# Performance work log

Hardware: AMD Instinct MI355X
Metric: run time of the kernel (lower is better)

Reference implementation:

```python
import jax, jax.numpy as jnp
import numpy as np

D_MODEL = 1024
N_LAYERS = 2
D_STATE = 16
D_CONV = 4
D_INNER = 2 * D_MODEL          # mamba expand=2
DT_RANK = 64                   # ceil(d_model/16)
EPS = 1e-5


def rmsnorm(x, w, eps=EPS):
    return x * jax.lax.rsqrt(jnp.mean(x * x, axis=-1, keepdims=True) + eps) * w


def silu(x):
    return x * jax.nn.sigmoid(x)


def selective_scan(u, dt, A, B, C, Dp):
    # u, dt: (b,l,d)  A: (d,n)  B,C: (b,l,n)  Dp: (d,)
    b, l, d = u.shape
    n = A.shape[1]

    def step(h, inp):
        u_t, dt_t, B_t, C_t = inp          # (b,d),(b,d),(b,n),(b,n)
        dA = jnp.exp(dt_t[..., None] * A)  # (b,d,n)
        h = dA * h + (dt_t * u_t)[..., None] * B_t[:, None, :]
        y = jnp.einsum('bdn,bn->bd', h, C_t)
        return h, y

    h0 = jnp.zeros((b, d, n), u.dtype)
    xs = (u.transpose(1, 0, 2), dt.transpose(1, 0, 2),
          B.transpose(1, 0, 2), C.transpose(1, 0, 2))
    _, ys = jax.lax.scan(step, h0, xs)
    return ys.transpose(1, 0, 2) + u * Dp


def mamba_mixer(x, in_w, conv_w, conv_b, xp_w, dt_w, dt_b, A_log, Dp, out_w):
    b, l, _ = x.shape
    xz = jnp.einsum('bld,ed->ble', x, in_w)        # (b,l,2*d_inner)
    xi, z = jnp.split(xz, 2, axis=-1)
    # depthwise causal conv1d, kernel D_CONV
    xp = jnp.pad(xi, ((0, 0), (D_CONV - 1, 0), (0, 0)))
    xc = conv_b + sum(xp[:, k:k + l, :] * conv_w[:, k] for k in range(D_CONV))
    xc = silu(xc)
    dbc = jnp.einsum('bld,ed->ble', xc, xp_w)      # (b,l,dt_rank+2n)
    dt_low = dbc[..., :DT_RANK]
    Bm = dbc[..., DT_RANK:DT_RANK + D_STATE]
    Cm = dbc[..., DT_RANK + D_STATE:]
    dt = jax.nn.softplus(jnp.einsum('blr,dr->bld', dt_low, dt_w) + dt_b)
    A = -jnp.exp(A_log)
    y = selective_scan(xc, dt, A, Bm, Cm, Dp)
    y = y * silu(z)
    return jnp.einsum('bld,od->blo', y, out_w)


def setup_inputs() -> dict:
    key = jax.random.key(0)
    ks = jax.random.split(key, 8)
    s = 0.02
    hidden_states = jax.random.normal(ks[0], (1, 2048, D_MODEL), jnp.float32)
    norm_w = jnp.ones((N_LAYERS, D_MODEL), jnp.float32)
    in_proj_w = jax.random.normal(ks[1], (N_LAYERS, 2 * D_INNER, D_MODEL), jnp.float32) * s
    conv_w = jax.random.normal(ks[2], (N_LAYERS, D_INNER, D_CONV), jnp.float32) * 0.2
    conv_b = jnp.zeros((N_LAYERS, D_INNER), jnp.float32)
    x_proj_w = jax.random.normal(ks[3], (N_LAYERS, DT_RANK + 2 * D_STATE, D_INNER), jnp.float32) * s
    dt_proj_w = jax.random.normal(ks[4], (N_LAYERS, D_INNER, DT_RANK), jnp.float32) * (DT_RANK ** -0.5)
    # softplus^{-1}(0.01) ~= -4.6 (mamba dt bias init regime)
    dt_proj_b = jnp.full((N_LAYERS, D_INNER), -4.6, jnp.float32) + \
        jax.random.normal(ks[5], (N_LAYERS, D_INNER), jnp.float32) * 0.1
    A_log = jnp.log(jnp.broadcast_to(
        jnp.arange(1, D_STATE + 1, dtype=jnp.float32), (N_LAYERS, D_INNER, D_STATE)))
    D_param = jnp.ones((N_LAYERS, D_INNER), jnp.float32)
    out_proj_w = jax.random.normal(ks[6], (N_LAYERS, D_MODEL, D_INNER), jnp.float32) * s
    norm_f_w = jnp.ones((D_MODEL,), jnp.float32)
    return {
        'hidden_states': hidden_states, 'norm_w': norm_w, 'in_proj_w': in_proj_w,
        'conv_w': conv_w, 'conv_b': conv_b, 'x_proj_w': x_proj_w,
        'dt_proj_w': dt_proj_w, 'dt_proj_b': dt_proj_b, 'A_log': A_log,
        'D_param': D_param, 'out_proj_w': out_proj_w, 'norm_f_w': norm_f_w,
    }


def reference(hidden_states, norm_w, in_proj_w, conv_w, conv_b, x_proj_w,
              dt_proj_w, dt_proj_b, A_log, D_param, out_proj_w, norm_f_w):
    h = hidden_states
    residual = None
    for i in range(N_LAYERS):
        # fused add + RMSNorm (prenorm): residual accumulates the stream
        residual = h if residual is None else h + residual
        hn = rmsnorm(residual, norm_w[i])
        h = mamba_mixer(hn, in_proj_w[i], conv_w[i], conv_b[i], x_proj_w[i],
                        dt_proj_w[i], dt_proj_b[i], A_log[i], D_param[i], out_proj_w[i])
    # final fused add + RMSNorm (prenorm=False)
    return rmsnorm(h + residual, norm_f_w)
```

## Files before the change

### kernel.cpp

```cpp
#include <hip/hip_runtime.h>
#include <math.h>

#define D_MODEL 1024
#define D_INNER 2048
#define DPROJ   96
#define DT_RANK 64
#define NSTATE  16
#define SEQ     2048
#define CL      16
#define NCH     (SEQ/CL)
#define SCAN_SEGS 4
#define SCAN_CPS  (NCH / SCAN_SEGS)
#define LOG2E   1.44269504088896340736f

typedef unsigned short ushort_t;
typedef short v8s __attribute__((ext_vector_type(8)));
typedef unsigned short u8s __attribute__((ext_vector_type(8)));
typedef float v4f __attribute__((ext_vector_type(4)));
typedef __attribute__((address_space(3))) unsigned int as3_u32;
typedef __attribute__((address_space(1))) unsigned int as1_u32;

__device__ __forceinline__ float silu_f(float x) { return x / (1.f + expf(-x)); }

__device__ __forceinline__ ushort_t f2bf(float f) {
  union { float f; unsigned u; } x; x.f = f;
  unsigned r = x.u + 0x7fffu + ((x.u >> 16) & 1u);
  return (ushort_t)(r >> 16);
}
__device__ __forceinline__ float bf2f(ushort_t b) {
  union { unsigned u; float f; } x; x.u = ((unsigned)b) << 16; return x.f;
}

__device__ __forceinline__ void gl_lds16(const ushort_t* g, ushort_t* l) {
  __builtin_amdgcn_global_load_lds((const as1_u32*)g, (as3_u32*)l, 16, 0, 0);
}

__global__ __launch_bounds__(256) void addrms_kernel(
    const float* __restrict__ a, const float* __restrict__ a2,
    const float* __restrict__ a3, const float* __restrict__ a4,
    const float* __restrict__ b,
    const float* __restrict__ w, float* __restrict__ res_out,
    float* __restrict__ xnf, ushort_t* __restrict__ xnb) {
  int t = blockIdx.x;
  int tid = threadIdx.x;
  float v[4];
  float ss = 0.f;
#pragma unroll
  for (int j = 0; j < 4; ++j) {
    int dcol = tid + j * 256;
    size_t off = (size_t)t * D_MODEL + dcol;
    float x = a[off];
    if (a2) x += a2[off];
    if (a3) x += a3[off];
    if (a4) x += a4[off];
    if (b) x += b[off];
    v[j] = x;
    ss += x * x;
  }
#pragma unroll
  for (int off = 32; off > 0; off >>= 1) ss += __shfl_down(ss, off);
  __shared__ float red[4];
  __shared__ float rmsv;
  int wid = tid >> 6, lane = tid & 63;
  if (lane == 0) red[wid] = ss;
  __syncthreads();
  if (tid == 0) {
    float s = red[0] + red[1] + red[2] + red[3];
    rmsv = rsqrtf(s / (float)D_MODEL + 1e-5f);
  }
  __syncthreads();
  float r = rmsv;
#pragma unroll
  for (int j = 0; j < 4; ++j) {
    int dcol = tid + j * 256;
    if (res_out) res_out[(size_t)t * D_MODEL + dcol] = v[j];
    float xn = v[j] * r * w[dcol];
    if (xnf) xnf[(size_t)t * D_MODEL + dcol] = xn;
    if (xnb) xnb[(size_t)t * D_MODEL + dcol] = f2bf(xn);
  }
}

__global__ __launch_bounds__(256) void f2bf_all_kernel(
    const float* __restrict__ s0, ushort_t* __restrict__ d0, int n0,
    const float* __restrict__ s1, ushort_t* __restrict__ d1, int n1,
    const float* __restrict__ s2, ushort_t* __restrict__ d2, int n2,
    const float* __restrict__ s3, ushort_t* __restrict__ d3, int n3) {
  int j = blockIdx.x * 256 + threadIdx.x;
  const float* s; ushort_t* d;
  if (j < n0) { s = s0; d = d0; }
  else {
    j -= n0;
    if (j < n1) { s = s1; d = d1; }
    else {
      j -= n1;
      if (j < n2) { s = s2; d = d2; }
      else {
        j -= n2;
        if (j >= n3) return;
        s = s3; d = d3;
      }
    }
  }
  float4 v = ((const float4*)s)[j];
  ushort4 o;
  o.x = f2bf(v.x); o.y = f2bf(v.y); o.z = f2bf(v.z); o.w = f2bf(v.w);
  ((ushort4*)d)[j] = o;
}

template <int SPLITK, bool CLAMPN, int EPI>
__global__ __launch_bounds__(256) void gemm_bt(
    const ushort_t* __restrict__ A, const ushort_t* __restrict__ B,
    void* __restrict__ Cv, const float* __restrict__ bias,
    const ushort_t* __restrict__ upack,
    int M, int N, int K, int lda, int ldb, int ldc) {
  __shared__ ushort_t As[2][128 * 32];
  __shared__ ushort_t Bs[2][128 * 32];
  int tid = threadIdx.x;

  int gx = gridDim.x, gy = gridDim.y;
  int nwg = gx * gy * gridDim.z;
  int phys = blockIdx.x + gx * (blockIdx.y + gy * blockIdx.z);
  int q = nwg >> 3, r = nwg & 7;
  int xcd = phys & 7, idx8 = phys >> 3;
  int lbid = (xcd < r ? xcd * (q + 1) : r * (q + 1) + (xcd - r) * q) + idx8;
  int bx = lbid % gx, by = (lbid / gx) % gy, bz = lbid / (gx * gy);

  int bm = by * 128;
  int bn = bx * 128;
  int kchunk = K / SPLITK;
  int k0 = bz * kchunk;
  int nk = kchunk / 32;

  int lane = tid & 63, wid = tid >> 6;
  int wr = wid >> 1, wc = wid & 1;
  int lr = lane & 15;
  int ko = (lane >> 4) * 8;

  int rs0 = wid * 16 + (lane >> 2);
  int segc = (lane & 3) * 8;

  auto stage = [&](int buf, int kt) {
#pragma unroll
    for (int s = 0; s < 2; ++s) {
      int r2 = s * 64 + rs0;
      int cc = kt + segc;
      gl_lds16(A + (size_t)(bm + r2) * lda + cc, &As[buf][s * 2048 + wid * 512]);
      int bc = bn + r2;
      if (CLAMPN) bc = min(bc, N - 1);
      gl_lds16(B + (size_t)bc * ldb + cc, &Bs[buf][s * 2048 + wid * 512]);
    }
  };

  v4f acc[4][4] = {};

  stage(0, k0);
  __syncthreads();
  int cur = 0;
  for (int it = 0; it < nk; ++it) {
    if (it + 1 < nk) stage(cur ^ 1, k0 + (it + 1) * 32);
    v8s a[4], b[4];
#pragma unroll
    for (int m = 0; m < 4; ++m)
      a[m] = *(const v8s*)&As[cur][(wr * 64 + m * 16 + lr) * 32 + ko];
#pragma unroll
    for (int n = 0; n < 4; ++n)
      b[n] = *(const v8s*)&Bs[cur][(wc * 64 + n * 16 + lr) * 32 + ko];
#pragma unroll
    for (int m = 0; m < 4; ++m)
#pragma unroll
      for (int n = 0; n < 4; ++n)
        acc[m][n] = __builtin_amdgcn_mfma_f32_16x16x32_bf16(a[m], b[n], acc[m][n], 0, 0, 0);
    __syncthreads();
    cur ^= 1;
  }

  float* Cf = (float*)Cv;
  ushort_t* Cb = (ushort_t*)Cv;
  unsigned* Cu = (unsigned*)Cv;
  if (SPLITK > 1) Cf += (size_t)bz * (size_t)M * (size_t)ldc;

#pragma unroll
  for (int m = 0; m < 4; ++m) {
#pragma unroll
    for (int n = 0; n < 4; ++n) {
      int gc = bn + wc * 64 + n * 16 + lr;
      if (gc >= N) continue;
      int gr0 = bm + wr * 64 + m * 16 + (lane >> 4) * 4;
      float bv = (EPI == 1 || EPI == 3) ? bias[gc] : 0.f;
#pragma unroll
      for (int j = 0; j < 4; ++j) {
        float val = acc[m][n][j];
        size_t idx = (size_t)(gr0 + j) * ldc + gc;
        if (EPI == 0) {
          Cf[idx] = val;
        } else if (EPI == 1) {
          float x = val + bv;
          x = fmaxf(x, 0.f) + log1pf(expf(-fabsf(x)));
          Cb[idx] = f2bf(x);
        } else if (EPI == 2) {
          Cb[idx] = f2bf(val);
        } else {
          float x = val + bv;
          x = fmaxf(x, 0.f) + log1pf(expf(-fabsf(x)));
          Cu[idx] = (unsigned)f2bf(x) | ((unsigned)upack[idx] << 16);
        }
      }
    }
  }
}

__global__ __launch_bounds__(256) void reduceN_kernel(
    const float* __restrict__ part, float* __restrict__ out,
    ushort_t* __restrict__ outb, int sz, int nparts) {
  int idx = blockIdx.x * 256 + threadIdx.x;
  if (idx >= sz) return;
  float s = 0.f;
  for (int p = 0; p < nparts; ++p) s += part[idx + (size_t)p * sz];
  if (out) out[idx] = s;
  if (outb) outb[idx] = f2bf(s);
}

__global__ __launch_bounds__(256) void conv_silu_kernel(
    const ushort_t* __restrict__ xzb, const float* __restrict__ cw,
    const float* __restrict__ cb, ushort_t* __restrict__ xcb) {
  int idx = blockIdx.x * 256 + threadIdx.x;
  int t = idx >> 9;
  int c = (idx & 511) * 4;
  float acc[4];
  float4 cbv = *(const float4*)&cb[c];
  acc[0] = cbv.x; acc[1] = cbv.y; acc[2] = cbv.z; acc[3] = cbv.w;
  float4 wv[4];
#pragma unroll
  for (int i = 0; i < 4; ++i) wv[i] = *(const float4*)&cw[(c + i) * 4];
#pragma unroll
  for (int k = 0; k < 4; ++k) {
    int ts = t - 3 + k;
    if (ts < 0) continue;
    ushort4 x = *(const ushort4*)&xzb[(size_t)ts * 4096 + c];
    acc[0] = fmaf(bf2f(x.x), ((const float*)&wv[0])[k], acc[0]);
    acc[1] = fmaf(bf2f(x.y), ((const float*)&wv[1])[k], acc[1]);
    acc[2] = fmaf(bf2f(x.z), ((const float*)&wv[2])[k], acc[2]);
    acc[3] = fmaf(bf2f(x.w), ((const float*)&wv[3])[k], acc[3]);
  }
  ushort4 o;
  o.x = f2bf(silu_f(acc[0]));
  o.y = f2bf(silu_f(acc[1]));
  o.z = f2bf(silu_f(acc[2]));
  o.w = f2bf(silu_f(acc[3]));
  *(ushort4*)&xcb[(size_t)t * D_INNER + c] = o;
}

__global__ __launch_bounds__(256) void scan_passA_kernel(
    const unsigned* __restrict__ dtu, const ushort_t* __restrict__ dbcb,
    const float* __restrict__ A_log,
    ushort_t* __restrict__ aprodb, ushort_t* __restrict__ hendb) {
  __shared__ float Bsh[CL][16];
  int c = blockIdx.x;
  int d = blockIdx.y * 256 + threadIdx.x;
  int t0 = c * CL;
  {
    int j = threadIdx.x;
    if (j < CL * 4) {
      int r = j >> 2, col = (j & 3) * 4;
      ushort4 v = *(const ushort4*)&dbcb[(size_t)(t0 + r) * DPROJ + DT_RANK + col];
      Bsh[r][col]     = bf2f(v.x);
      Bsh[r][col + 1] = bf2f(v.y);
      Bsh[r][col + 2] = bf2f(v.z);
      Bsh[r][col + 3] = bf2f(v.w);
    }
  }
  float Av[NSTATE], h[NSTATE], ap[NSTATE];
#pragma unroll
  for (int n = 0; n < NSTATE; ++n) {
    Av[n] = -expf(A_log[(size_t)d * NSTATE + n]) * LOG2E;
    h[n] = 0.f;
    ap[n] = 1.f;
  }
  __syncthreads();
#pragma unroll 2
  for (int tt = 0; tt < CL; ++tt) {
    unsigned p = dtu[(size_t)(t0 + tt) * D_INNER + d];
    float dtv = bf2f((ushort_t)(p & 0xffffu));
    float uv  = bf2f((ushort_t)(p >> 16));
    float du = dtv * uv;
#pragma unroll
    for (int n = 0; n < NSTATE; ++n) {
      float dA = exp2f(dtv * Av[n]);
      h[n] = fmaf(dA, h[n], du * Bsh[tt][n]);
      ap[n] *= dA;
    }
  }
  size_t base = ((size_t)c * D_INNER + d) * NSTATE;
  u8s oa, ob, ha, hb;
#pragma unroll
  for (int n = 0; n < 8; ++n) {
    oa[n] = f2bf(ap[n]);     ob[n] = f2bf(ap[n + 8]);
    ha[n] = f2bf(h[n]);      hb[n] = f2bf(h[n + 8]);
  }
  *(u8s*)&aprodb[base] = oa;     *(u8s*)&aprodb[base + 8] = ob;
  *(u8s*)&hendb[base]  = ha;     *(u8s*)&hendb[base + 8]  = hb;
}

__global__ __launch_bounds__(256) void scan_passB_kernel(
    const ushort_t* __restrict__ aprodb, ushort_t* __restrict__ hendb) {
  int tid = threadIdx.x;
  int lane = tid & 63;
  int wave = tid >> 6;
  int seg = lane >> 4;
  int chain = blockIdx.x * 64 + wave * 16 + (lane & 15);
  const size_t stride = (size_t)D_INNER * NSTATE;
  float a[SCAN_CPS], e[SCAN_CPS];
  float P = 1.f, E = 0.f;
  int c0 = seg * SCAN_CPS;
#pragma unroll
  for (int j = 0; j < SCAN_CPS; ++j) {
    a[j] = bf2f(aprodb[(size_t)(c0 + j) * stride + chain]);
    e[j] = bf2f(hendb[(size_t)(c0 + j) * stride + chain]);
    E = fmaf(a[j], E, e[j]);
    P *= a[j];
  }
#pragma unroll
  for (int dstep = 1; dstep < SCAN_SEGS; dstep <<= 1) {
    float Pp = __shfl_up(P, dstep * 16);
    float Ep = __shfl_up(E, dstep * 16);
    if (seg >= dstep) { E = fmaf(P, Ep, E); P *= Pp; }
  }
  float Ex = __shfl_up(E, 16);
  if (seg == 0) Ex = 0.f;
  float h = Ex;
#pragma unroll
  for (int j = 0; j < SCAN_CPS; ++j) {
    hendb[(size_t)(c0 + j) * stride + chain] = f2bf(h);
    h = fmaf(a[j], h, e[j]);
  }
}

__global__ __launch_bounds__(256) void scan_passC_kernel(
    const unsigned* __restrict__ dtu, const ushort_t* __restrict__ dbcb,
    const float* __restrict__ A_log, const float* __restrict__ Dp,
    const ushort_t* __restrict__ xzb, const ushort_t* __restrict__ hinb,
    ushort_t* __restrict__ yb) {
  __shared__ float BCsh[CL][32];
  int c = blockIdx.x;
  int d = blockIdx.y * 256 + threadIdx.x;
  int t0 = c * CL;
  {
    int j = threadIdx.x;
    if (j < CL * 8) {
      int r = j >> 3, col = (j & 7) * 4;
      ushort4 v = *(const ushort4*)&dbcb[(size_t)(t0 + r) * DPROJ + DT_RANK + col];
      BCsh[r][col]     = bf2f(v.x);
      BCsh[r][col + 1] = bf2f(v.y);
      BCsh[r][col + 2] = bf2f(v.z);
      BCsh[r][col + 3] = bf2f(v.w);
    }
  }
  float Av[NSTATE], h[NSTATE];
  size_t base = ((size_t)c * D_INNER + d) * NSTATE;
  u8s h0 = *(const u8s*)&hinb[base];
  u8s h1 = *(const u8s*)&hinb[base + 8];
#pragma unroll
  for (int n = 0; n < NSTATE; ++n) {
    Av[n] = -expf(A_log[(size_t)d * NSTATE + n]) * LOG2E;
    h[n] = (n < 8) ? bf2f(h0[n & 7]) : bf2f(h1[n & 7]);
  }
  float Dv = Dp[d];
  __syncthreads();
#pragma unroll 2
  for (int tt = 0; tt < CL; ++tt) {
    unsigned p = dtu[(size_t)(t0 + tt) * D_INNER + d];
    float dtv = bf2f((ushort_t)(p & 0xffffu));
    float uv  = bf2f((ushort_t)(p >> 16));
    float du = dtv * uv;
    float yv = 0.f;
#pragma unroll
    for (int n = 0; n < NSTATE; ++n) {
      float dA = exp2f(dtv * Av[n]);
      h[n] = fmaf(dA, h[n], du * BCsh[tt][n]);
      yv = fmaf(h[n], BCsh[tt][16 + n], yv);
    }
    float zv = bf2f(xzb[(size_t)(t0 + tt) * 4096 + D_INNER + d]);
    yb[(size_t)(t0 + tt) * D_INNER + d] = f2bf((yv + uv * Dv) * silu_f(zv));
  }
}

extern "C" void kernel_launch(void* const* d_in, const int* in_sizes, int n_in,
                              void* d_out, int out_size, void* d_ws, size_t ws_size,
                              hipStream_t stream) {
  const float* h_in   = (const float*)d_in[0];
  const float* norm_w = (const float*)d_in[1];
  const float* in_w   = (const float*)d_in[2];
  const float* conv_w = (const float*)d_in[3];
  const float* conv_b = (const float*)d_in[4];
  const float* xp_w   = (const float*)d_in[5];
  const float* dt_w   = (const float*)d_in[6];
  const float* dt_b   = (const float*)d_in[7];
  const float* A_log  = (const float*)d_in[8];
  const float* Dp     = (const float*)d_in[9];
  const float* out_w  = (const float*)d_in[10];
  const float* normf  = (const float*)d_in[11];
  float* out = (float*)d_out;

  float* ws = (float*)d_ws;
  const size_t TD = (size_t)SEQ * D_MODEL;
  const size_t TI = (size_t)SEQ * D_INNER;
  const size_t ST = (size_t)NCH * D_INNER * NSTATE;
  const size_t DB = (size_t)SEQ * DPROJ;
  const size_t INW = (size_t)2 * D_INNER * D_MODEL;
  const size_t XPW = (size_t)DPROJ * D_INNER;
  const size_t DTW = (size_t)D_INNER * DT_RANK;
  const size_t OUW = (size_t)D_MODEL * D_INNER;

  float* res = ws; ws += TD;
  float* pk  = ws; ws += 4 * TD;
  unsigned* dtu = (unsigned*)ws; ws += TI;
  ushort_t* aprodb = (ushort_t*)ws;
  ushort_t* hendb  = aprodb + ST;
  ushort_t* hnb  = hendb + ST;
  ushort_t* xzb  = hnb + TD;
  ushort_t* xcb  = xzb + 2 * TI;
  ushort_t* ybf  = xcb + TI;
  ushort_t* dbcb = ybf + TI;
  ushort_t* inwb = dbcb + DB;
  ushort_t* xpwb = inwb + 2 * INW;
  ushort_t* dtwb = xpwb + 2 * XPW;
  ushort_t* ouwb = dtwb + 2 * DTW;

  {
    int n0 = (int)(2 * INW / 4), n1 = (int)(2 * XPW / 4);
    int n2 = (int)(2 * DTW / 4), n3 = (int)(2 * OUW / 4);
    int tot = n0 + n1 + n2 + n3;
    f2bf_all_kernel<<<(tot + 255) / 256, 256, 0, stream>>>(
        in_w, inwb, n0, xp_w, xpwb, n1, dt_w, dtwb, n2, out_w, ouwb, n3);
  }

  for (int i = 0; i < 2; ++i) {
    addrms_kernel<<<SEQ, 256, 0, stream>>>(
        i == 0 ? h_in : pk,
        i == 0 ? nullptr : pk + TD,
        i == 0 ? nullptr : pk + 2 * TD,
        i == 0 ? nullptr : pk + 3 * TD,
        i == 0 ? nullptr : res,
        norm_w + (size_t)i * D_MODEL, res, nullptr, hnb);
    gemm_bt<1, false, 2><<<dim3(32, 16, 1), 256, 0, stream>>>(
        hnb, inwb + (size_t)i * INW, xzb, nullptr, nullptr,
        SEQ, 2 * D_INNER, D_MODEL, D_MODEL, D_MODEL, 2 * D_INNER);
    conv_silu_kernel<<<(int)(TI / 4 / 256), 256, 0, stream>>>(
        xzb, conv_w + (size_t)i * D_INNER * 4, conv_b + (size_t)i * D_INNER, xcb);
    gemm_bt<16, true, 0><<<dim3(1, 16, 16), 256, 0, stream>>>(
        xcb, xpwb + (size_t)i * XPW, pk, nullptr, nullptr,
        SEQ, DPROJ, D_INNER, D_INNER, D_INNER, DPROJ);
    reduceN_kernel<<<(DB + 255) / 256, 256, 0, stream>>>(
        pk, nullptr, dbcb, (int)DB, 16);
    gemm_bt<1, false, 3><<<dim3(16, 16, 1), 256, 0, stream>>>(
        dbcb, dtwb + (size_t)i * DTW, dtu, dt_b + (size_t)i * D_INNER, xcb,
        SEQ, D_INNER, DT_RANK, DPROJ, DT_RANK, D_INNER);
    scan_passA_kernel<<<dim3(NCH, D_INNER / 256), 256, 0, stream>>>(
        dtu, dbcb, A_log + (size_t)i * D_INNER * NSTATE, aprodb, hendb);
    scan_passB_kernel<<<(D_INNER * NSTATE) / 64, 256, 0, stream>>>(aprodb, hendb);
    scan_passC_kernel<<<dim3(NCH, D_INNER / 256), 256, 0, stream>>>(
        dtu, dbcb, A_log + (size_t)i * D_INNER * NSTATE,
        Dp + (size_t)i * D_INNER, xzb, hendb, ybf);
    gemm_bt<4, false, 0><<<dim3(8, 16, 4), 256, 0, stream>>>(
        ybf, ouwb + (size_t)i * OUW, pk, nullptr, nullptr,
        SEQ, D_MODEL, D_INNER, D_INNER, D_INNER, D_MODEL);
  }
  addrms_kernel<<<SEQ, 256, 0, stream>>>(
      pk, pk + TD, pk + 2 * TD, pk + 3 * TD, res, normf, nullptr, out, nullptr);
}
```

Before: 368.0 us.

## Store split-K partials in bf16 and process four timesteps per conv thread

The split-K partial outputs of the out_proj and x_proj GEMMs are now written as bf16 rather than fp32. The reduce kernel and the add+RMSNorm kernel read and sum these bf16 partials, which halves the partial-buffer write and read traffic. The depthwise conv kernel now computes four consecutive timesteps per thread from seven loaded rows, so each input row is loaded fewer times and a quarter as many threads are launched. Rounding the partials to bf16 before summing adds precision loss to the residual stream and to the dt/B/C projections.

```diff
diff --git a/kernel.cpp b/kernel.cpp
--- a/kernel.cpp
+++ b/kernel.cpp
@@ -12,6 +12,7 @@
 #define SCAN_SEGS 4
 #define SCAN_CPS  (NCH / SCAN_SEGS)
 #define LOG2E   1.44269504088896340736f
+#define TDC     ((size_t)SEQ * D_MODEL)
 
 typedef unsigned short ushort_t;
 typedef short v8s __attribute__((ext_vector_type(8)));
@@ -36,8 +37,7 @@
 }
 
 __global__ __launch_bounds__(256) void addrms_kernel(
-    const float* __restrict__ a, const float* __restrict__ a2,
-    const float* __restrict__ a3, const float* __restrict__ a4,
+    const float* __restrict__ a, const ushort_t* __restrict__ p4,
     const float* __restrict__ b,
     const float* __restrict__ w, float* __restrict__ res_out,
     float* __restrict__ xnf, ushort_t* __restrict__ xnb) {
@@ -49,10 +49,13 @@
   for (int j = 0; j < 4; ++j) {
     int dcol = tid + j * 256;
     size_t off = (size_t)t * D_MODEL + dcol;
-    float x = a[off];
-    if (a2) x += a2[off];
-    if (a3) x += a3[off];
-    if (a4) x += a4[off];
+    float x;
+    if (p4) {
+      x = bf2f(p4[off]) + bf2f(p4[off + TDC]) +
+          bf2f(p4[off + 2 * TDC]) + bf2f(p4[off + 3 * TDC]);
+    } else {
+      x = a[off];
+    }
     if (b) x += b[off];
     v[j] = x;
     ss += x * x;
@@ -177,7 +180,7 @@
   float* Cf = (float*)Cv;
   ushort_t* Cb = (ushort_t*)Cv;
   unsigned* Cu = (unsigned*)Cv;
-  if (SPLITK > 1) Cf += (size_t)bz * (size_t)M * (size_t)ldc;
+  size_t zoff = (SPLITK > 1) ? (size_t)bz * (size_t)M * (size_t)ldc : 0;
 
 #pragma unroll
   for (int m = 0; m < 4; ++m) {
@@ -190,7 +193,7 @@
 #pragma unroll
       for (int j = 0; j < 4; ++j) {
         float val = acc[m][n][j];
-        size_t idx = (size_t)(gr0 + j) * ldc + gc;
+        size_t idx = zoff + (size_t)(gr0 + j) * ldc + gc;
         if (EPI == 0) {
           Cf[idx] = val;
         } else if (EPI == 1) {
@@ -209,45 +212,55 @@
   }
 }
 
-__global__ __launch_bounds__(256) void reduceN_kernel(
-    const float* __restrict__ part, float* __restrict__ out,
-    ushort_t* __restrict__ outb, int sz, int nparts) {
+__global__ __launch_bounds__(256) void reduceNb_kernel(
+    const ushort_t* __restrict__ part, ushort_t* __restrict__ outb,
+    int sz, int nparts) {
   int idx = blockIdx.x * 256 + threadIdx.x;
   if (idx >= sz) return;
   float s = 0.f;
-  for (int p = 0; p < nparts; ++p) s += part[idx + (size_t)p * sz];
-  if (out) out[idx] = s;
-  if (outb) outb[idx] = f2bf(s);
+  for (int p = 0; p < nparts; ++p) s += bf2f(part[idx + (size_t)p * sz]);
+  outb[idx] = f2bf(s);
 }
 
 __global__ __launch_bounds__(256) void conv_silu_kernel(
     const ushort_t* __restrict__ xzb, const float* __restrict__ cw,
     const float* __restrict__ cb, ushort_t* __restrict__ xcb) {
   int idx = blockIdx.x * 256 + threadIdx.x;
-  int t = idx >> 9;
+  int tq = idx >> 9;
   int c = (idx & 511) * 4;
-  float acc[4];
+  int t0 = tq * 4;
   float4 cbv = *(const float4*)&cb[c];
-  acc[0] = cbv.x; acc[1] = cbv.y; acc[2] = cbv.z; acc[3] = cbv.w;
   float4 wv[4];
 #pragma unroll
   for (int i = 0; i < 4; ++i) wv[i] = *(const float4*)&cw[(c + i) * 4];
-#pragma unroll
-  for (int k = 0; k < 4; ++k) {
-    int ts = t - 3 + k;
-    if (ts < 0) continue;
-    ushort4 x = *(const ushort4*)&xzb[(size_t)ts * 4096 + c];
-    acc[0] = fmaf(bf2f(x.x), ((const float*)&wv[0])[k], acc[0]);
-    acc[1] = fmaf(bf2f(x.y), ((const float*)&wv[1])[k], acc[1]);
-    acc[2] = fmaf(bf2f(x.z), ((const float*)&wv[2])[k], acc[2]);
-    acc[3] = fmaf(bf2f(x.w), ((const float*)&wv[3])[k], acc[3]);
-  }
-  ushort4 o;
-  o.x = f2bf(silu_f(acc[0]));
-  o.y = f2bf(silu_f(acc[1]));
-  o.z = f2bf(silu_f(acc[2]));
-  o.w = f2bf(silu_f(acc[3]));
-  *(ushort4*)&xcb[(size_t)t * D_INNER + c] = o;
+  float rows[7][4];
+#pragma unroll
+  for (int k = 0; k < 7; ++k) {
+    int ts = t0 - 3 + k;
+    if (ts < 0) {
+      rows[k][0] = rows[k][1] = rows[k][2] = rows[k][3] = 0.f;
+    } else {
+      ushort4 x = *(const ushort4*)&xzb[(size_t)ts * 4096 + c];
+      rows[k][0] = bf2f(x.x); rows[k][1] = bf2f(x.y);
+      rows[k][2] = bf2f(x.z); rows[k][3] = bf2f(x.w);
+    }
+  }
+#pragma unroll
+  for (int j = 0; j < 4; ++j) {
+    float acc[4] = {cbv.x, cbv.y, cbv.z, cbv.w};
+#pragma unroll
+    for (int k = 0; k < 4; ++k) {
+#pragma unroll
+      for (int i = 0; i < 4; ++i)
+        acc[i] = fmaf(rows[j + k][i], ((const float*)&wv[i])[k], acc[i]);
+    }
+    ushort4 o;
+    o.x = f2bf(silu_f(acc[0]));
+    o.y = f2bf(silu_f(acc[1]));
+    o.z = f2bf(silu_f(acc[2]));
+    o.w = f2bf(silu_f(acc[3]));
+    *(ushort4*)&xcb[(size_t)(t0 + j) * D_INNER + c] = o;
+  }
 }
 
 __global__ __launch_bounds__(256) void scan_passA_kernel(
@@ -412,19 +425,20 @@
   const size_t OUW = (size_t)D_MODEL * D_INNER;
 
   float* res = ws; ws += TD;
-  float* pk  = ws; ws += 4 * TD;
+  ushort_t* pkb = (ushort_t*)ws; ws += 2 * TD;
   unsigned* dtu = (unsigned*)ws; ws += TI;
-  ushort_t* aprodb = (ushort_t*)ws;
-  ushort_t* hendb  = aprodb + ST;
-  ushort_t* hnb  = hendb + ST;
-  ushort_t* xzb  = hnb + TD;
-  ushort_t* xcb  = xzb + 2 * TI;
-  ushort_t* ybf  = xcb + TI;
-  ushort_t* dbcb = ybf + TI;
-  ushort_t* inwb = dbcb + DB;
-  ushort_t* xpwb = inwb + 2 * INW;
-  ushort_t* dtwb = xpwb + 2 * XPW;
-  ushort_t* ouwb = dtwb + 2 * DTW;
+  ushort_t* us = (ushort_t*)ws;
+  ushort_t* aprodb = us;  us += ST;
+  ushort_t* hendb  = us;  us += ST;
+  ushort_t* hnb  = us;    us += TD;
+  ushort_t* xzb  = us;    us += 2 * TI;
+  ushort_t* xcb  = us;    us += TI;
+  ushort_t* ybf  = us;    us += TI;
+  ushort_t* dbcb = us;    us += DB;
+  ushort_t* inwb = us;    us += 2 * INW;
+  ushort_t* xpwb = us;    us += 2 * XPW;
+  ushort_t* dtwb = us;    us += 2 * DTW;
+  ushort_t* ouwb = us;    us += 2 * OUW;
 
   {
     int n0 = (int)(2 * INW / 4), n1 = (int)(2 * XPW / 4);
@@ -436,22 +450,18 @@
 
   for (int i = 0; i < 2; ++i) {
     addrms_kernel<<<SEQ, 256, 0, stream>>>(
-        i == 0 ? h_in : pk,
-        i == 0 ? nullptr : pk + TD,
-        i == 0 ? nullptr : pk + 2 * TD,
-        i == 0 ? nullptr : pk + 3 * TD,
+        h_in, i == 0 ? nullptr : pkb,
         i == 0 ? nullptr : res,
         norm_w + (size_t)i * D_MODEL, res, nullptr, hnb);
     gemm_bt<1, false, 2><<<dim3(32, 16, 1), 256, 0, stream>>>(
         hnb, inwb + (size_t)i * INW, xzb, nullptr, nullptr,
         SEQ, 2 * D_INNER, D_MODEL, D_MODEL, D_MODEL, 2 * D_INNER);
-    conv_silu_kernel<<<(int)(TI / 4 / 256), 256, 0, stream>>>(
+    conv_silu_kernel<<<(int)(TI / 16 / 256), 256, 0, stream>>>(
         xzb, conv_w + (size_t)i * D_INNER * 4, conv_b + (size_t)i * D_INNER, xcb);
-    gemm_bt<16, true, 0><<<dim3(1, 16, 16), 256, 0, stream>>>(
-        xcb, xpwb + (size_t)i * XPW, pk, nullptr, nullptr,
+    gemm_bt<16, true, 2><<<dim3(1, 16, 16), 256, 0, stream>>>(
+        xcb, xpwb + (size_t)i * XPW, pkb, nullptr, nullptr,
         SEQ, DPROJ, D_INNER, D_INNER, D_INNER, DPROJ);
-    reduceN_kernel<<<(DB + 255) / 256, 256, 0, stream>>>(
-        pk, nullptr, dbcb, (int)DB, 16);
+    reduceNb_kernel<<<(DB + 255) / 256, 256, 0, stream>>>(pkb, dbcb, (int)DB, 16);
     gemm_bt<1, false, 3><<<dim3(16, 16, 1), 256, 0, stream>>>(
         dbcb, dtwb + (size_t)i * DTW, dtu, dt_b + (size_t)i * D_INNER, xcb,
         SEQ, D_INNER, DT_RANK, DPROJ, DT_RANK, D_INNER);
@@ -461,10 +471,10 @@
     scan_passC_kernel<<<dim3(NCH, D_INNER / 256), 256, 0, stream>>>(
         dtu, dbcb, A_log + (size_t)i * D_INNER * NSTATE,
         Dp + (size_t)i * D_INNER, xzb, hendb, ybf);
-    gemm_bt<4, false, 0><<<dim3(8, 16, 4), 256, 0, stream>>>(
-        ybf, ouwb + (size_t)i * OUW, pk, nullptr, nullptr,
+    gemm_bt<4, false, 2><<<dim3(8, 16, 4), 256, 0, stream>>>(
+        ybf, ouwb + (size_t)i * OUW, pkb, nullptr, nullptr,
         SEQ, D_MODEL, D_INNER, D_INNER, D_INNER, D_MODEL);
   }
   addrms_kernel<<<SEQ, 256, 0, stream>>>(
-      pk, pk + TD, pk + 2 * TD, pk + 3 * TD, res, normf, nullptr, out, nullptr);
-}
+      h_in, pkb, res, normf, nullptr, out, nullptr);
+}
```

New measurement: 349.1 us. -5.1%, faster.
